# Performance work log

Measured on AMD Instinct MI355X. Metric: run time of the kernel, lower is better.

The kernel has to match this reference:

```python
import jax, jax.numpy as jnp
import numpy as np

B, N, D, H, HD, C = 2, 2048, 2048, 16, 128, 128  # batch, seq, embed, heads, head_dim, chunk
EPS = 1e-6


def setup_inputs() -> dict:
    key = jax.random.key(0)
    ks = jax.random.split(key, 9)
    s = 0.02
    x = jax.random.normal(ks[0], (B, N, D), jnp.float32)
    # per-head negative log decay (lambda = exp(log_decay) in (0,1))
    log_decay = -jax.random.uniform(ks[1], (H,), jnp.float32, minval=0.01, maxval=1.0)
    Wq = jax.random.normal(ks[2], (D, D), jnp.float32) * s
    Wk = jax.random.normal(ks[3], (D, D), jnp.float32) * s
    Wv = jax.random.normal(ks[4], (D, D), jnp.float32) * s
    Wo = jax.random.normal(ks[5], (D, D), jnp.float32) * s
    Wg1 = jax.random.normal(ks[6], (D, HD), jnp.float32) * s
    Wg2 = jax.random.normal(ks[7], (HD, D), jnp.float32) * s
    norm_w = jnp.ones((D,), jnp.float32)
    return dict(x=x, log_decay=log_decay, Wq=Wq, Wk=Wk, Wv=Wv, Wo=Wo,
                Wg1=Wg1, Wg2=Wg2, norm_w=norm_w)


def _lasd(q, k, v, ld):
    # causal linear attention with per-head scalar log-decay, chunked scan.
    # q,k,v: [B,N,H,HD]; ld: [H] (negative). Recurrence: S_t = exp(ld)*S_{t-1} + k_t v_t^T; o_t = q_t @ S_t
    nc = N // C
    to_chunks = lambda t: t.reshape(B, nc, C, H, HD).transpose(1, 0, 3, 2, 4)  # [nc,B,H,C,HD]
    qc, kc, vc = map(to_chunks, (q, k, v))
    i = jnp.arange(C, dtype=jnp.float32)
    diff = i[:, None] - i[None, :]                     # [C,C]
    Dm = jnp.exp(jnp.where(diff >= 0, ld[:, None, None] * diff, -jnp.inf))  # [H,C,C]
    dq = jnp.exp(ld[:, None] * (i + 1.0))              # [H,C] decay applied to q vs chunk-start state
    dk = jnp.exp(ld[:, None] * (C - 1.0 - i))          # [H,C] decay applied to k for state update
    dS = jnp.exp(ld * C)                               # [H]   chunk-level state decay

    def step(S, qkv):
        qb, kb, vb = qkv                               # [B,H,C,HD]
        attn = jnp.einsum('bhid,bhjd->bhij', qb, kb) * Dm
        o = jnp.einsum('bhij,bhje->bhie', attn, vb)
        o = o + jnp.einsum('bhid,bhde->bhie', qb * dq[None, :, :, None], S)
        S = S * dS[None, :, None, None] + jnp.einsum('bhjd,bhje->bhde', kb * dk[None, :, :, None], vb)
        return S, o

    S0 = jnp.zeros((B, H, HD, HD), jnp.float32)
    _, o = jax.lax.scan(step, S0, (qc, kc, vc))        # [nc,B,H,C,HD]
    return o.transpose(1, 0, 3, 2, 4).reshape(B, N, H, HD)


def reference(x, log_decay, Wq, Wk, Wv, Wo, Wg1, Wg2, norm_w):
    silu = jax.nn.silu
    q = silu(x @ Wq).reshape(B, N, H, HD)
    k = silu(x @ Wk).reshape(B, N, H, HD)
    v = silu(x @ Wv).reshape(B, N, H, HD)
    o = _lasd(q, k, v, log_decay).reshape(B, N, D)
    gate = jax.nn.sigmoid((x @ Wg1) @ Wg2)             # two stacked linears, no nonlinearity between
    o = o * gate
    o = o * jax.lax.rsqrt(jnp.mean(o * o, axis=-1, keepdims=True) + EPS) * norm_w  # rmsnorm
    return o @ Wo
```

## Files before the change

### kernel.cpp

```cpp
#include <hip/hip_runtime.h>
#include <hip/hip_bf16.h>
#include <cstdint>
#include <cstddef>

#define B_   2
#define N_   2048
#define D_   2048
#define H_   16
#define HD_  128
#define C_   128
#define NC_  16
#define M_   4096
#define QKVG_ 8192

typedef __attribute__((ext_vector_type(8))) short bf16x8;
typedef __attribute__((ext_vector_type(4))) float f32x4;
typedef __attribute__((ext_vector_type(16))) float f32x16;

__device__ __forceinline__ uint16_t f2bf(float f){
  __hip_bfloat16 h = __float2bfloat16(f);
  return *reinterpret_cast<uint16_t*>(&h);
}
__device__ __forceinline__ float bf2f(uint16_t u){
  union { uint32_t i; float f; } v; v.i = ((uint32_t)u) << 16; return v.f;
}

__device__ __forceinline__ void async16(const uint16_t* g, uint16_t* l){
  __builtin_amdgcn_global_load_lds(
      (const __attribute__((address_space(1))) void*)g,
      (__attribute__((address_space(3))) void*)l, 16, 0, 0);
}

__device__ __forceinline__ int swz(int row, int c){
  return row*128 + ((((c >> 3) ^ row) & 15) << 3) + (c & 7);
}

__global__ __launch_bounds__(256) void cast_kernel(
    const float* __restrict__ x, uint16_t* __restrict__ y)
{
  int i = (blockIdx.x*256 + threadIdx.x)*4;
  float4 f = *(const float4*)(x + i);
  ushort4 u;
  u.x = f2bf(f.x); u.y = f2bf(f.y); u.z = f2bf(f.z); u.w = f2bf(f.w);
  *(ushort4*)(y + i) = u;
}

__global__ __launch_bounds__(256)
void prep_weights(const float* __restrict__ Wq, const float* __restrict__ Wk,
                  const float* __restrict__ Wv, const float* __restrict__ Wo,
                  const float* __restrict__ Wg2, const float* __restrict__ Wg1,
                  uint16_t* __restrict__ WT, uint16_t* __restrict__ WoT,
                  uint16_t* __restrict__ Wg2T, uint16_t* __restrict__ Wg1b)
{
  const int z = blockIdx.z;
  const int tx = threadIdx.x & 31;
  const int ty = threadIdx.x >> 5;
  __shared__ uint16_t tile[32][33];

  if (z == 5){
    if (blockIdx.x >= 4) return;
    const int r0 = blockIdx.y*32, c0 = blockIdx.x*32;
    #pragma unroll
    for (int rr = 0; rr < 4; ++rr){
      int r = r0 + ty + rr*8;
      Wg1b[(size_t)r*HD_ + c0 + tx] = f2bf(Wg1[(size_t)r*HD_ + c0 + tx]);
    }
    return;
  }

  const float* src; uint16_t* dst; int R, Cc;
  if (z < 3)      { src = (z==0)?Wq:(z==1)?Wk:Wv; dst = WT + (size_t)z*D_*D_; R = D_; Cc = D_; }
  else if (z == 3){ src = Wo;  dst = WoT;  R = D_;  Cc = D_; }
  else            { if (blockIdx.y >= 4) return;
                    src = Wg2; dst = Wg2T; R = HD_; Cc = D_; }

  const int r0 = blockIdx.y*32, c0 = blockIdx.x*32;
  #pragma unroll
  for (int rr = 0; rr < 4; ++rr){
    int r = ty + rr*8;
    tile[r][tx] = f2bf(src[(size_t)(r0 + r)*Cc + c0 + tx]);
  }
  __syncthreads();
  #pragma unroll
  for (int rr = 0; rr < 4; ++rr){
    int r = ty + rr*8;
    dst[(size_t)(c0 + r)*R + r0 + tx] = tile[tx][r];
  }
}

template<int ACT, int OUTBF>
__global__ __launch_bounds__(256)
void gemm_bt2(const uint16_t* __restrict__ A, const uint16_t* __restrict__ Bt,
              void* __restrict__ Cout, int M, int Ncols, int K, int klen)
{
  __shared__ __align__(16) uint16_t As[128*64];
  __shared__ __align__(16) uint16_t Bs[128*64];
  const int t    = threadIdx.x;
  const int lane = t & 63, wave = t >> 6;
  const int wm = wave >> 1, wn = wave & 1;
  const int row0 = wm*64, col0 = wn*64;
  const int lm = lane & 31, lh = lane >> 5;

  const uint16_t* Ap = A  + (size_t)(blockIdx.y*128)*K;
  const uint16_t* Bp = Bt + (size_t)(blockIdx.x*128)*K;
  const int kbeg = blockIdx.z * klen;

  f32x16 acc[2][2];
  #pragma unroll
  for (int i = 0; i < 2; ++i)
    #pragma unroll
    for (int j = 0; j < 2; ++j)
      #pragma unroll
      for (int r = 0; r < 16; ++r) acc[i][j][r] = 0.f;

  const int srow = t >> 3;
  const int gch  = (t & 7) ^ (srow & 7);
  const size_t aoff0 = (size_t)srow*K + gch*8;

  for (int k0 = kbeg; k0 < kbeg + klen; k0 += 64){
    #pragma unroll
    for (int c = 0; c < 4; ++c){
      async16(Ap + (size_t)(c*32)*K + aoff0 + k0, As + c*2048 + t*8);
      async16(Bp + (size_t)(c*32)*K + aoff0 + k0, Bs + c*2048 + t*8);
    }
    __syncthreads();
    #pragma unroll
    for (int kh = 0; kh < 4; ++kh){
      bf16x8 af[2], bfr[2];
      const int ch = kh*2 + lh;
      #pragma unroll
      for (int i = 0; i < 2; ++i){
        int r = row0 + i*32 + lm;
        af[i] = *(const bf16x8*)(As + r*64 + ((ch ^ (r & 7)) << 3));
      }
      #pragma unroll
      for (int j = 0; j < 2; ++j){
        int r = col0 + j*32 + lm;
        bfr[j] = *(const bf16x8*)(Bs + r*64 + ((ch ^ (r & 7)) << 3));
      }
      #pragma unroll
      for (int i = 0; i < 2; ++i)
        #pragma unroll
        for (int j = 0; j < 2; ++j)
          acc[i][j] = __builtin_amdgcn_mfma_f32_32x32x16_bf16(af[i], bfr[j], acc[i][j], 0, 0, 0);
    }
    __syncthreads();
  }

  const int mode = (ACT == 3) ? ((blockIdx.x < 48) ? 1 : 2) : ACT;
  uint16_t* outb = (uint16_t*)Cout;
  float*    outf = (float*)Cout + (OUTBF ? 0 : (size_t)blockIdx.z*M*Ncols);
  #pragma unroll
  for (int i = 0; i < 2; ++i){
    #pragma unroll
    for (int j = 0; j < 2; ++j){
      #pragma unroll
      for (int r = 0; r < 16; ++r){
        int row = blockIdx.y*128 + row0 + i*32 + (r & 3) + 8*(r >> 2) + 4*lh;
        int col = blockIdx.x*128 + col0 + j*32 + lm;
        float v = acc[i][j][r];
        if (mode == 1)      v = v / (1.f + __expf(-v));
        else if (mode == 2) v = 1.f / (1.f + __expf(-v));
        size_t off = (size_t)row*Ncols + col;
        if (OUTBF) outb[off] = f2bf(v);
        else       outf[off] = v;
      }
    }
  }
}

template<int ACT, int OUTBF>
__global__ __launch_bounds__(512, 2)
void gemm256(const uint16_t* __restrict__ A, const uint16_t* __restrict__ Bt,
             void* __restrict__ Cout, int M, int Ncols, int K, int klen)
{
  __shared__ __align__(16) uint16_t As[2*256*32];
  __shared__ __align__(16) uint16_t Bs[2*256*32];
  const int t    = threadIdx.x;
  const int lane = t & 63, wave = t >> 6;
  const int wm = wave >> 1, wn = wave & 1;
  const int lm = lane & 31, lh = lane >> 5;
  const int sl0 = (lh ^ ((lm >> 1) & 3)) << 3;
  const int ar = wm*64  + lm;
  const int br = wn*128 + lm;

  const uint16_t* Ap = A  + (size_t)(blockIdx.y*256)*K;
  const uint16_t* Bp = Bt + (size_t)(blockIdx.x*256)*K;
  const int kbeg = blockIdx.z*klen;
  const int NT   = klen >> 5;

  const int r_lo = t >> 2;
  const int gch  = (t & 3) ^ ((r_lo >> 1) & 3);
  const size_t src0 = (size_t)r_lo*K + gch*8;
  const size_t src1 = src0 + (size_t)128*K;
  const int ldst = t*8;

  f32x16 acc[2][4];
  #pragma unroll
  for (int i = 0; i < 2; ++i)
    #pragma unroll
    for (int j = 0; j < 4; ++j)
      #pragma unroll
      for (int r = 0; r < 16; ++r) acc[i][j][r] = 0.f;

  async16(Ap + src0 + kbeg,      As + ldst);
  async16(Ap + src1 + kbeg,      As + 4096 + ldst);
  async16(Bp + src0 + kbeg,      Bs + ldst);
  async16(Bp + src1 + kbeg,      Bs + 4096 + ldst);
  async16(Ap + src0 + kbeg + 32, As + 8192 + ldst);
  async16(Ap + src1 + kbeg + 32, As + 8192 + 4096 + ldst);
  async16(Bp + src0 + kbeg + 32, Bs + 8192 + ldst);
  async16(Bp + src1 + kbeg + 32, Bs + 8192 + 4096 + ldst);
  asm volatile("s_waitcnt vmcnt(4)" ::: "memory");
  __builtin_amdgcn_s_barrier();
  asm volatile("" ::: "memory");

  bf16x8 af0[2], bf0[4], af1[2], bf1[4];
  #pragma unroll
  for (int i = 0; i < 2; ++i) af0[i] = *(const bf16x8*)(As + (ar + i*32)*32 + sl0);
  #pragma unroll
  for (int j = 0; j < 4; ++j) bf0[j] = *(const bf16x8*)(Bs + (br + j*32)*32 + sl0);

  for (int tt = 0; tt < NT; ++tt){
    uint16_t* Ac = As + (tt & 1)*8192;
    uint16_t* Bc = Bs + (tt & 1)*8192;
    const uint16_t* An = As + ((tt & 1) ^ 1)*8192;
    const uint16_t* Bn = Bs + ((tt & 1) ^ 1)*8192;

    #pragma unroll
    for (int i = 0; i < 2; ++i) af1[i] = *(const bf16x8*)(Ac + (ar + i*32)*32 + (sl0 ^ 16));
    #pragma unroll
    for (int j = 0; j < 4; ++j) bf1[j] = *(const bf16x8*)(Bc + (br + j*32)*32 + (sl0 ^ 16));
    __builtin_amdgcn_s_setprio(1);
    #pragma unroll
    for (int i = 0; i < 2; ++i)
      #pragma unroll
      for (int j = 0; j < 4; ++j)
        acc[i][j] = __builtin_amdgcn_mfma_f32_32x32x16_bf16(af0[i], bf0[j], acc[i][j], 0, 0, 0);
    __builtin_amdgcn_s_setprio(0);
    asm volatile("s_waitcnt lgkmcnt(0)" ::: "memory");
    __builtin_amdgcn_s_barrier();
    asm volatile("" ::: "memory");

    if (tt + 2 < NT){
      const size_t kc = (size_t)kbeg + (size_t)(tt + 2)*32;
      async16(Ap + src0 + kc, Ac + ldst);
      async16(Ap + src1 + kc, Ac + 4096 + ldst);
      async16(Bp + src0 + kc, Bc + ldst);
      async16(Bp + src1 + kc, Bc + 4096 + ldst);
      asm volatile("s_waitcnt vmcnt(4)" ::: "memory");
    } else {
      asm volatile("s_waitcnt vmcnt(0)" ::: "memory");
    }
    __builtin_amdgcn_s_barrier();
    asm volatile("" ::: "memory");
    if (tt + 1 < NT){
      #pragma unroll
      for (int i = 0; i < 2; ++i) af0[i] = *(const bf16x8*)(An + (ar + i*32)*32 + sl0);
      #pragma unroll
      for (int j = 0; j < 4; ++j) bf0[j] = *(const bf16x8*)(Bn + (br + j*32)*32 + sl0);
    }
    __builtin_amdgcn_s_setprio(1);
    #pragma unroll
    for (int i = 0; i < 2; ++i)
      #pragma unroll
      for (int j = 0; j < 4; ++j)
        acc[i][j] = __builtin_amdgcn_mfma_f32_32x32x16_bf16(af1[i], bf1[j], acc[i][j], 0, 0, 0);
    __builtin_amdgcn_s_setprio(0);
  }

  const int mode = (ACT == 3) ? (((blockIdx.x << 8) < Ncols - 2048) ? 1 : 2) : ACT;
  uint16_t* outb = (uint16_t*)Cout;
  float*    outf = (float*)Cout + (OUTBF ? 0 : (size_t)blockIdx.z*M*Ncols);
  #pragma unroll
  for (int i = 0; i < 2; ++i){
    #pragma unroll
    for (int j = 0; j < 4; ++j){
      #pragma unroll
      for (int r = 0; r < 16; ++r){
        int row = blockIdx.y*256 + wm*64  + i*32 + (r & 3) + 8*(r >> 2) + 4*lh;
        int col = blockIdx.x*256 + wn*128 + j*32 + lm;
        float v = acc[i][j][r];
        if (mode == 1)      v = v / (1.f + __expf(-v));
        else if (mode == 2) v = 1.f / (1.f + __expf(-v));
        size_t off = (size_t)row*Ncols + col;
        if (OUTBF) outb[off] = f2bf(v);
        else       outf[off] = v;
      }
    }
  }
}

__global__ __launch_bounds__(256)
void add_kernel(const float* __restrict__ p0, const float* __restrict__ p1,
                float* __restrict__ out)
{
  int i = (blockIdx.x*256 + threadIdx.x)*4;
  float4 a = *(const float4*)(p0 + i);
  float4 b = *(const float4*)(p1 + i);
  float4 o; o.x = a.x+b.x; o.y = a.y+b.y; o.z = a.z+b.z; o.w = a.w+b.w;
  *(float4*)(out + i) = o;
}

__global__ __launch_bounds__(256)
void chunk_state_kernel(const uint16_t* __restrict__ qkvg,
                        const float* __restrict__ log_decay, uint16_t* __restrict__ MsumT)
{
  __shared__ __align__(16) uint16_t vT[128*128];
  __shared__ __align__(16) uint16_t kT[128*128];
  const int h = blockIdx.x, b = blockIdx.y, ic = blockIdx.z;
  const int t    = threadIdx.x;
  const int lane = t & 63, wave = t >> 6;
  const int wm = wave >> 1, wn = wave & 1;
  const int e0 = wm*64, d0 = wn*64;
  const int lr = lane & 15, kq = lane >> 4;
  const float ld = log_decay[h];
  const size_t rowbase = (size_t)b*N_ + (size_t)ic*C_;
  const uint16_t* kb = qkvg + (size_t)D_;
  const uint16_t* vb = qkvg + (size_t)2*D_;

  #pragma unroll 4
  for (int it = 0; it < 64; ++it){
    int idx = t + it*256;
    int j = idx >> 7, e = idx & 127;
    uint16_t vv = vb[(rowbase + j)*QKVG_ + h*HD_ + e];
    float kf = bf2f(kb[(rowbase + j)*QKVG_ + h*HD_ + e]) * __expf(ld * (float)(C_ - 1 - j));
    vT[swz(e, j)] = vv;
    kT[swz(e, j)] = f2bf(kf);
  }
  __syncthreads();

  const f32x4 zero = {0.f, 0.f, 0.f, 0.f};
  f32x4 acc[4][4];
  #pragma unroll
  for (int i = 0; i < 4; ++i)
    #pragma unroll
    for (int j = 0; j < 4; ++j) acc[i][j] = zero;

  #pragma unroll
  for (int kt = 0; kt < 4; ++kt){
    bf16x8 af[4], bfr[4];
    #pragma unroll
    for (int i = 0; i < 4; ++i)
      af[i]  = *(const bf16x8*)(vT + swz(e0 + i*16 + lr, kt*32 + kq*8));
    #pragma unroll
    for (int j = 0; j < 4; ++j)
      bfr[j] = *(const bf16x8*)(kT + swz(d0 + j*16 + lr, kt*32 + kq*8));
    #pragma unroll
    for (int i = 0; i < 4; ++i)
      #pragma unroll
      for (int j = 0; j < 4; ++j)
        acc[i][j] = __builtin_amdgcn_mfma_f32_16x16x32_bf16(af[i], bfr[j], acc[i][j], 0, 0, 0);
  }

  uint16_t* Mout = MsumT + (((size_t)ic*B_ + b)*H_ + h)*(size_t)(HD_*HD_);
  #pragma unroll
  for (int i = 0; i < 4; ++i)
    #pragma unroll
    for (int j = 0; j < 4; ++j)
      #pragma unroll
      for (int r = 0; r < 4; ++r)
        Mout[(size_t)(e0 + i*16 + kq*4 + r)*HD_ + d0 + j*16 + lr] = f2bf(acc[i][j][r]);
}

__global__ __launch_bounds__(256)
void scan_kernel(const uint16_t* __restrict__ MsumT, const float* __restrict__ log_decay,
                 uint16_t* __restrict__ StT)
{
  const int h = blockIdx.x, b = blockIdx.y;
  const float ld = log_decay[h];
  const float dS = __expf(ld * (float)C_);
  const int base_e = blockIdx.z*2048;
  float cur[8];
  #pragma unroll
  for (int r = 0; r < 8; ++r) cur[r] = 0.f;
  for (int i = 0; i < NC_; ++i){
    const size_t base = (((size_t)i*B_ + b)*H_ + h)*(size_t)(HD_*HD_) + base_e;
    #pragma unroll
    for (int r = 0; r < 8; ++r){
      int idx = threadIdx.x + r*256;
      StT[base + idx] = f2bf(cur[r]);
      cur[r] = cur[r]*dS + bf2f(MsumT[base + idx]);
    }
  }
}

__global__ __launch_bounds__(256)
void attn_kernel(const uint16_t* __restrict__ qkvg, const uint16_t* __restrict__ StT,
                 const float* __restrict__ log_decay, float* __restrict__ o_attn)
{
  __shared__ __align__(16) uint16_t Ps[128*128];
  __shared__ __align__(16) uint16_t vT[128*128];
  const int h = blockIdx.x, b = blockIdx.y, ic = blockIdx.z;
  const int t    = threadIdx.x;
  const int lane = t & 63, wave = t >> 6;
  const int wm = wave >> 1, wn = wave & 1;
  const int row0 = wm*64, col0 = wn*64;
  const int lr = lane & 15, kq = lane >> 4;
  const float ld = log_decay[h];
  const size_t rowbase = (size_t)b*N_ + (size_t)ic*C_;
  const uint16_t* qb = qkvg;
  const uint16_t* kb = qkvg + (size_t)D_;
  const uint16_t* vb = qkvg + (size_t)2*D_;

  #pragma unroll 4
  for (int it = 0; it < 64; ++it){
    int idx = t + it*256;
    int j = idx >> 7, e = idx & 127;
    vT[swz(e, j)] = vb[(rowbase + j)*QKVG_ + h*HD_ + e];
  }

  const f32x4 zero = {0.f, 0.f, 0.f, 0.f};
  f32x4 acc[4][4];
  #pragma unroll
  for (int i = 0; i < 4; ++i)
    #pragma unroll
    for (int j = 0; j < 4; ++j) acc[i][j] = zero;

  #pragma unroll
  for (int kt = 0; kt < 4; ++kt){
    bf16x8 af[4], bfr[4];
    #pragma unroll
    for (int i = 0; i < 4; ++i)
      af[i]  = *(const bf16x8*)(qb + (rowbase + row0 + i*16 + lr)*QKVG_ + h*HD_ + kt*32 + kq*8);
    #pragma unroll
    for (int j = 0; j < 4; ++j)
      bfr[j] = *(const bf16x8*)(kb + (rowbase + col0 + j*16 + lr)*QKVG_ + h*HD_ + kt*32 + kq*8);
    #pragma unroll
    for (int i = 0; i < 4; ++i)
      #pragma unroll
      for (int j = 0; j < 4; ++j)
        acc[i][j] = __builtin_amdgcn_mfma_f32_16x16x32_bf16(af[i], bfr[j], acc[i][j], 0, 0, 0);
  }
  #pragma unroll
  for (int i = 0; i < 4; ++i)
    #pragma unroll
    for (int j = 0; j < 4; ++j)
      #pragma unroll
      for (int r = 0; r < 4; ++r){
        int row = row0 + i*16 + kq*4 + r;
        int col = col0 + j*16 + lr;
        int dlt = row - col;
        float f = (dlt >= 0) ? __expf(ld * (float)dlt) : 0.f;
        Ps[swz(row, col)] = f2bf(acc[i][j][r] * f);
      }

  #pragma unroll
  for (int i = 0; i < 4; ++i)
    #pragma unroll
    for (int j = 0; j < 4; ++j) acc[i][j] = zero;
  const uint16_t* Sb = StT + (((size_t)ic*B_ + b)*H_ + h)*(size_t)(HD_*HD_);
  #pragma unroll
  for (int kt = 0; kt < 4; ++kt){
    bf16x8 af[4], bfr[4];
    #pragma unroll
    for (int i = 0; i < 4; ++i)
      af[i]  = *(const bf16x8*)(qb + (rowbase + row0 + i*16 + lr)*QKVG_ + h*HD_ + kt*32 + kq*8);
    #pragma unroll
    for (int j = 0; j < 4; ++j)
      bfr[j] = *(const bf16x8*)(Sb + (size_t)(col0 + j*16 + lr)*HD_ + kt*32 + kq*8);
    #pragma unroll
    for (int i = 0; i < 4; ++i)
      #pragma unroll
      for (int j = 0; j < 4; ++j)
        acc[i][j] = __builtin_amdgcn_mfma_f32_16x16x32_bf16(af[i], bfr[j], acc[i][j], 0, 0, 0);
  }
  #pragma unroll
  for (int i = 0; i < 4; ++i)
    #pragma unroll
    for (int r = 0; r < 4; ++r){
      float dqv = __expf(ld * (float)(row0 + i*16 + kq*4 + r + 1));
      #pragma unroll
      for (int j = 0; j < 4; ++j) acc[i][j][r] *= dqv;
    }

  __syncthreads();

  #pragma unroll
  for (int kt = 0; kt < 4; ++kt){
    bf16x8 af[4], bfr[4];
    #pragma unroll
    for (int i = 0; i < 4; ++i)
      af[i]  = *(const bf16x8*)(Ps + swz(row0 + i*16 + lr, kt*32 + kq*8));
    #pragma unroll
    for (int j = 0; j < 4; ++j)
      bfr[j] = *(const bf16x8*)(vT + swz(col0 + j*16 + lr, kt*32 + kq*8));
    #pragma unroll
    for (int i = 0; i < 4; ++i)
      #pragma unroll
      for (int j = 0; j < 4; ++j)
        acc[i][j] = __builtin_amdgcn_mfma_f32_16x16x32_bf16(af[i], bfr[j], acc[i][j], 0, 0, 0);
  }

  #pragma unroll
  for (int i = 0; i < 4; ++i)
    #pragma unroll
    for (int j = 0; j < 4; ++j)
      #pragma unroll
      for (int r = 0; r < 4; ++r){
        int row = row0 + i*16 + kq*4 + r;
        int col = col0 + j*16 + lr;
        o_attn[(rowbase + row)*D_ + h*HD_ + col] = acc[i][j][r];
      }
}

__global__ __launch_bounds__(256)
void gate_norm_kernel(const float* __restrict__ o_attn, const uint16_t* __restrict__ qkvg,
                      const float* __restrict__ norm_w, uint16_t* __restrict__ on)
{
  const int row = blockIdx.x;
  const int t = threadIdx.x;
  const int c1 = t*4, c2 = 1024 + t*4;
  const float*    orow = o_attn + (size_t)row*D_;
  const uint16_t* grow = qkvg + (size_t)row*QKVG_ + 3*D_;
  float4  o1 = *(const float4*)(orow + c1);
  float4  o2 = *(const float4*)(orow + c2);
  ushort4 g1 = *(const ushort4*)(grow + c1);
  ushort4 g2 = *(const ushort4*)(grow + c2);
  float v[8];
  v[0] = o1.x*bf2f(g1.x); v[1] = o1.y*bf2f(g1.y); v[2] = o1.z*bf2f(g1.z); v[3] = o1.w*bf2f(g1.w);
  v[4] = o2.x*bf2f(g2.x); v[5] = o2.y*bf2f(g2.y); v[6] = o2.z*bf2f(g2.z); v[7] = o2.w*bf2f(g2.w);
  float s = 0.f;
  #pragma unroll
  for (int k = 0; k < 8; ++k) s += v[k]*v[k];
  #pragma unroll
  for (int off = 32; off > 0; off >>= 1) s += __shfl_down(s, off);
  __shared__ float red[4];
  if ((t & 63) == 0) red[t >> 6] = s;
  __syncthreads();
  float total = red[0] + red[1] + red[2] + red[3];
  float scale = rsqrtf(total * (1.f/(float)D_) + 1e-6f);
  float4 w1 = *(const float4*)(norm_w + c1);
  float4 w2 = *(const float4*)(norm_w + c2);
  ushort4 b1, b2;
  b1.x = f2bf(v[0]*scale*w1.x); b1.y = f2bf(v[1]*scale*w1.y);
  b1.z = f2bf(v[2]*scale*w1.z); b1.w = f2bf(v[3]*scale*w1.w);
  b2.x = f2bf(v[4]*scale*w2.x); b2.y = f2bf(v[5]*scale*w2.y);
  b2.z = f2bf(v[6]*scale*w2.z); b2.w = f2bf(v[7]*scale*w2.w);
  *(ushort4*)(on + (size_t)row*D_ + c1) = b1;
  *(ushort4*)(on + (size_t)row*D_ + c2) = b2;
}

extern "C" void kernel_launch(void* const* d_in, const int* in_sizes, int n_in,
                              void* d_out, int out_size, void* d_ws, size_t ws_size,
                              hipStream_t stream) {
  const float* x         = (const float*)d_in[0];
  const float* log_decay = (const float*)d_in[1];
  const float* Wq        = (const float*)d_in[2];
  const float* Wk        = (const float*)d_in[3];
  const float* Wv        = (const float*)d_in[4];
  const float* Wo        = (const float*)d_in[5];
  const float* Wg1       = (const float*)d_in[6];
  const float* Wg2       = (const float*)d_in[7];
  const float* norm_w    = (const float*)d_in[8];
  float* out = (float*)d_out;

  uint8_t* p = (uint8_t*)d_ws;
  uint16_t* xb    = (uint16_t*)p; p += (size_t)M_*D_*2;
  uint16_t* WT    = (uint16_t*)p; p += (size_t)QKVG_*D_*2;
  uint16_t* WoT   = (uint16_t*)p; p += (size_t)D_*D_*2;
  uint16_t* Wg1b  = (uint16_t*)p; p += (size_t)D_*HD_*2;
  uint16_t* Wg2T  = (uint16_t*)p; p += (size_t)D_*HD_*2;
  uint16_t* qkvg  = (uint16_t*)p; p += (size_t)M_*QKVG_*2;
  uint16_t* MsumT = (uint16_t*)p; p += (size_t)NC_*B_*H_*HD_*HD_*2;
  uint16_t* StT   = (uint16_t*)p; p += (size_t)NC_*B_*H_*HD_*HD_*2;
  float*    o_att = (float*)WT;
  uint16_t* on    = xb;
  float*    part  = (float*)qkvg;

  cast_kernel<<<(M_*D_)/1024, 256, 0, stream>>>(x, xb);
  prep_weights<<<dim3(64, 64, 6), 256, 0, stream>>>(Wq, Wk, Wv, Wo, Wg2, Wg1,
                                                    WT, WoT, Wg2T, Wg1b);

  gemm_bt2<0,1><<<dim3(D_/128, D_/128, 1), 256, 0, stream>>>(
      Wg2T, Wg1b, WT + (size_t)3*D_*D_, D_, D_, HD_, HD_);

  gemm256<3,1><<<dim3(QKVG_/256, M_/256, 1), 512, 0, stream>>>(
      xb, WT, qkvg, M_, QKVG_, D_, D_);

  chunk_state_kernel<<<dim3(H_, B_, NC_), 256, 0, stream>>>(qkvg, log_decay, MsumT);
  scan_kernel<<<dim3(H_, B_, 8), 256, 0, stream>>>(MsumT, log_decay, StT);
  attn_kernel<<<dim3(H_, B_, NC_), 256, 0, stream>>>(qkvg, StT, log_decay, o_att);

  gate_norm_kernel<<<M_, 256, 0, stream>>>(o_att, qkvg, norm_w, on);
  gemm256<0,0><<<dim3(D_/256, M_/256, 2), 512, 0, stream>>>(
      on, WoT, part, M_, D_, D_, D_/2);
  add_kernel<<<(M_*D_)/1024, 256, 0, stream>>>(part, part + (size_t)M_*D_, out);
}
```

Baseline: 454.6 us.

## Deepen gemm256 K-tile to 64 and remap waves to 2x4 layout

```diff
diff --git a/kernel.cpp b/kernel.cpp
--- a/kernel.cpp
+++ b/kernel.cpp
@@ -174,81 +174,98 @@
 void gemm256(const uint16_t* __restrict__ A, const uint16_t* __restrict__ Bt,
              void* __restrict__ Cout, int M, int Ncols, int K, int klen)
 {
-  __shared__ __align__(16) uint16_t As[2*256*32];
-  __shared__ __align__(16) uint16_t Bs[2*256*32];
+  __shared__ __align__(16) uint16_t As[2*256*64];
+  __shared__ __align__(16) uint16_t Bs[2*256*64];
   const int t    = threadIdx.x;
   const int lane = t & 63, wave = t >> 6;
-  const int wm = wave >> 1, wn = wave & 1;
+  const int wm = wave >> 2, wn = wave & 3;
   const int lm = lane & 31, lh = lane >> 5;
-  const int sl0 = (lh ^ ((lm >> 1) & 3)) << 3;
-  const int ar = wm*64  + lm;
-  const int br = wn*128 + lm;
+
+  int arow[4], brow[2], sl[4];
+  #pragma unroll
+  for (int m = 0; m < 4; ++m) arow[m] = (wm*128 + m*32 + lm)*64;
+  #pragma unroll
+  for (int n = 0; n < 2; ++n) brow[n] = (wn*64 + n*32 + lm)*64;
+  #pragma unroll
+  for (int kk = 0; kk < 4; ++kk) sl[kk] = ((kk*2 + lh) ^ (lm & 7)) << 3;
 
   const uint16_t* Ap = A  + (size_t)(blockIdx.y*256)*K;
   const uint16_t* Bp = Bt + (size_t)(blockIdx.x*256)*K;
   const int kbeg = blockIdx.z*klen;
-  const int NT   = klen >> 5;
-
-  const int r_lo = t >> 2;
-  const int gch  = (t & 3) ^ ((r_lo >> 1) & 3);
-  const size_t src0 = (size_t)r_lo*K + gch*8;
-  const size_t src1 = src0 + (size_t)128*K;
+  const int NT   = klen >> 6;
+
+  const int r64  = t >> 3;
+  const int gch  = (t & 7) ^ (r64 & 7);
+  const size_t srcoff = (size_t)r64*K + gch*8;
   const int ldst = t*8;
 
-  f32x16 acc[2][4];
-  #pragma unroll
-  for (int i = 0; i < 2; ++i)
-    #pragma unroll
-    for (int j = 0; j < 4; ++j)
-      #pragma unroll
-      for (int r = 0; r < 16; ++r) acc[i][j][r] = 0.f;
-
-  async16(Ap + src0 + kbeg,      As + ldst);
-  async16(Ap + src1 + kbeg,      As + 4096 + ldst);
-  async16(Bp + src0 + kbeg,      Bs + ldst);
-  async16(Bp + src1 + kbeg,      Bs + 4096 + ldst);
-  async16(Ap + src0 + kbeg + 32, As + 8192 + ldst);
-  async16(Ap + src1 + kbeg + 32, As + 8192 + 4096 + ldst);
-  async16(Bp + src0 + kbeg + 32, Bs + 8192 + ldst);
-  async16(Bp + src1 + kbeg + 32, Bs + 8192 + 4096 + ldst);
-  asm volatile("s_waitcnt vmcnt(4)" ::: "memory");
+  f32x16 acc[4][2];
+  #pragma unroll
+  for (int m = 0; m < 4; ++m)
+    #pragma unroll
+    for (int n = 0; n < 2; ++n)
+      #pragma unroll
+      for (int r = 0; r < 16; ++r) acc[m][n][r] = 0.f;
+
+  auto stageA = [&](size_t kofs, int lb){
+    #pragma unroll
+    for (int s = 0; s < 4; ++s)
+      async16(Ap + (size_t)(s*64)*K + srcoff + kofs, As + lb + s*4096 + ldst);
+  };
+  auto stageB = [&](size_t kofs, int lb){
+    #pragma unroll
+    for (int s = 0; s < 4; ++s)
+      async16(Bp + (size_t)(s*64)*K + srcoff + kofs, Bs + lb + s*4096 + ldst);
+  };
+
+  stageA(kbeg, 0);        stageB(kbeg, 0);
+  stageA(kbeg + 64, 16384); stageB(kbeg + 64, 16384);
+  asm volatile("s_waitcnt vmcnt(8)" ::: "memory");
   __builtin_amdgcn_s_barrier();
   asm volatile("" ::: "memory");
 
-  bf16x8 af0[2], bf0[4], af1[2], bf1[4];
-  #pragma unroll
-  for (int i = 0; i < 2; ++i) af0[i] = *(const bf16x8*)(As + (ar + i*32)*32 + sl0);
-  #pragma unroll
-  for (int j = 0; j < 4; ++j) bf0[j] = *(const bf16x8*)(Bs + (br + j*32)*32 + sl0);
+  bf16x8 afA[4], afB[4], bfr[2][4];
+  #pragma unroll
+  for (int kk = 0; kk < 4; ++kk) afA[kk] = *(const bf16x8*)(As + arow[0] + sl[kk]);
+
+  #define MFMA8(AF, MI) do {                                                   \
+    __builtin_amdgcn_s_setprio(1);                                             \
+    _Pragma("unroll") for (int n = 0; n < 2; ++n)                              \
+      _Pragma("unroll") for (int kk = 0; kk < 4; ++kk)                         \
+        acc[MI][n] = __builtin_amdgcn_mfma_f32_32x32x16_bf16(                  \
+            AF[kk], bfr[n][kk], acc[MI][n], 0, 0, 0);                          \
+    __builtin_amdgcn_s_setprio(0); } while(0)
 
   for (int tt = 0; tt < NT; ++tt){
-    uint16_t* Ac = As + (tt & 1)*8192;
-    uint16_t* Bc = Bs + (tt & 1)*8192;
-    const uint16_t* An = As + ((tt & 1) ^ 1)*8192;
-    const uint16_t* Bn = Bs + ((tt & 1) ^ 1)*8192;
-
-    #pragma unroll
-    for (int i = 0; i < 2; ++i) af1[i] = *(const bf16x8*)(Ac + (ar + i*32)*32 + (sl0 ^ 16));
-    #pragma unroll
-    for (int j = 0; j < 4; ++j) bf1[j] = *(const bf16x8*)(Bc + (br + j*32)*32 + (sl0 ^ 16));
-    __builtin_amdgcn_s_setprio(1);
-    #pragma unroll
-    for (int i = 0; i < 2; ++i)
-      #pragma unroll
-      for (int j = 0; j < 4; ++j)
-        acc[i][j] = __builtin_amdgcn_mfma_f32_32x32x16_bf16(af0[i], bf0[j], acc[i][j], 0, 0, 0);
-    __builtin_amdgcn_s_setprio(0);
+    const int cb = (tt & 1)*16384, nb = cb ^ 16384;
+    const uint16_t* Ac = As + cb;
+    const uint16_t* Bc = Bs + cb;
+    const uint16_t* An = As + nb;
+
+    #pragma unroll
+    for (int n = 0; n < 2; ++n)
+      #pragma unroll
+      for (int kk = 0; kk < 4; ++kk)
+        bfr[n][kk] = *(const bf16x8*)(Bc + brow[n] + sl[kk]);
+    #pragma unroll
+    for (int kk = 0; kk < 4; ++kk) afB[kk] = *(const bf16x8*)(Ac + arow[1] + sl[kk]);
+    MFMA8(afA, 0);
+
+    #pragma unroll
+    for (int kk = 0; kk < 4; ++kk) afA[kk] = *(const bf16x8*)(Ac + arow[2] + sl[kk]);
+    MFMA8(afB, 1);
+
+    #pragma unroll
+    for (int kk = 0; kk < 4; ++kk) afB[kk] = *(const bf16x8*)(Ac + arow[3] + sl[kk]);
+    MFMA8(afA, 2);
     asm volatile("s_waitcnt lgkmcnt(0)" ::: "memory");
     __builtin_amdgcn_s_barrier();
     asm volatile("" ::: "memory");
 
     if (tt + 2 < NT){
-      const size_t kc = (size_t)kbeg + (size_t)(tt + 2)*32;
-      async16(Ap + src0 + kc, Ac + ldst);
-      async16(Ap + src1 + kc, Ac + 4096 + ldst);
-      async16(Bp + src0 + kc, Bc + ldst);
-      async16(Bp + src1 + kc, Bc + 4096 + ldst);
-      asm volatile("s_waitcnt vmcnt(4)" ::: "memory");
+      const size_t kc = (size_t)kbeg + (size_t)(tt + 2)*64;
+      stageA(kc, cb); stageB(kc, cb);
+      asm volatile("s_waitcnt vmcnt(8)" ::: "memory");
     } else {
       asm volatile("s_waitcnt vmcnt(0)" ::: "memory");
     }
@@ -256,31 +273,24 @@
     asm volatile("" ::: "memory");
     if (tt + 1 < NT){
       #pragma unroll
-      for (int i = 0; i < 2; ++i) af0[i] = *(const bf16x8*)(An + (ar + i*32)*32 + sl0);
-      #pragma unroll
-      for (int j = 0; j < 4; ++j) bf0[j] = *(const bf16x8*)(Bn + (br + j*32)*32 + sl0);
-    }
-    __builtin_amdgcn_s_setprio(1);
-    #pragma unroll
-    for (int i = 0; i < 2; ++i)
-      #pragma unroll
-      for (int j = 0; j < 4; ++j)
-        acc[i][j] = __builtin_amdgcn_mfma_f32_32x32x16_bf16(af1[i], bf1[j], acc[i][j], 0, 0, 0);
-    __builtin_amdgcn_s_setprio(0);
-  }
+      for (int kk = 0; kk < 4; ++kk) afA[kk] = *(const bf16x8*)(An + arow[0] + sl[kk]);
+    }
+    MFMA8(afB, 3);
+  }
+  #undef MFMA8
 
   const int mode = (ACT == 3) ? (((blockIdx.x << 8) < Ncols - 2048) ? 1 : 2) : ACT;
   uint16_t* outb = (uint16_t*)Cout;
   float*    outf = (float*)Cout + (OUTBF ? 0 : (size_t)blockIdx.z*M*Ncols);
   #pragma unroll
-  for (int i = 0; i < 2; ++i){
-    #pragma unroll
-    for (int j = 0; j < 4; ++j){
+  for (int m = 0; m < 4; ++m){
+    #pragma unroll
+    for (int n = 0; n < 2; ++n){
       #pragma unroll
       for (int r = 0; r < 16; ++r){
-        int row = blockIdx.y*256 + wm*64  + i*32 + (r & 3) + 8*(r >> 2) + 4*lh;
-        int col = blockIdx.x*256 + wn*128 + j*32 + lm;
-        float v = acc[i][j][r];
+        int row = blockIdx.y*256 + wm*128 + m*32 + (r & 3) + 8*(r >> 2) + 4*lh;
+        int col = blockIdx.x*256 + wn*64  + n*32 + lm;
+        float v = acc[m][n][r];
         if (mode == 1)      v = v / (1.f + __expf(-v));
         else if (mode == 2) v = 1.f / (1.f + __expf(-v));
         size_t off = (size_t)row*Ncols + col;
```

New measurement: 425.0 us. 6.5% less time.
